# Kernel tuning notes

Hardware: AMD Instinct MI355X
Metric: run time of the kernel (lower is better)

Reference implementation:

```python
import jax, jax.numpy as jnp
import numpy as np
import math


def setup_inputs() -> dict:
    key = jax.random.key(0)
    k_x, k_q, k_k, k_v, k_o = jax.random.split(key, 5)
    B, S, D_IN, H, D_K, D_V, D_OUT = 1, 4096, 512, 8, 64, 64, 512
    # torch.rand -> uniform[0,1); scaled by 0.02 to keep softmax unsaturated
    scale = 0.02
    return {
        "x": jax.random.normal(k_x, (B, S, D_IN), dtype=jnp.float32),
        "W_q": jax.random.uniform(k_q, (H, D_IN, D_K), dtype=jnp.float32) * scale,
        "W_k": jax.random.uniform(k_k, (H, D_IN, D_K), dtype=jnp.float32) * scale,
        "W_v": jax.random.uniform(k_v, (H, D_IN, D_V), dtype=jnp.float32) * scale,
        "W_o": jax.random.uniform(k_o, (H, D_V, D_OUT), dtype=jnp.float32) * scale,
    }


def reference(x, W_q, W_k, W_v, W_o):
    # x: [B,S,d_in]; W_q/W_k: [H,d_in,d_k]; W_v: [H,d_in,d_v]; W_o: [H,d_v,d_out]
    S = x.shape[-2]
    d_key = W_k.shape[-1]
    Q = jnp.einsum('hjk,blj->bhlk', W_q, x)   # [B,H,S,d_k]
    K = jnp.einsum('hjk,blj->bhlk', W_k, x)   # [B,H,S,d_k]
    V = jnp.einsum('hjk,blj->bhlk', W_v, x)   # [B,H,S,d_v]
    # causal mask: True where masked (strict upper triangle)
    mask = jnp.triu(jnp.ones((S, S), dtype=bool), k=1)  # [S,S]
    scores = jnp.einsum('bhik,bhjk->bhij', Q, K)        # [B,H,S,S]
    scores = jnp.where(mask, -jnp.inf, scores)
    # is_scaled=True: divide by sqrt(d_key) before softmax
    weights = jax.nn.softmax(scores / math.sqrt(d_key), axis=-1)
    weights = jnp.where(mask, 0.0, weights)
    values = jnp.einsum('bhij,bhjv->bhiv', weights, V)  # [B,H,S,d_v]
    return jnp.einsum('hvk,bhlv->blk', W_o, values)     # [B,S,d_out]
```

## Files before the change

### kernel.cpp

```cpp
#include <hip/hip_runtime.h>
#include <hip/hip_bf16.h>
#include <math.h>

#define S_LEN 4096
#define NH    8

typedef __attribute__((ext_vector_type(8))) short bf16x8;
typedef __attribute__((ext_vector_type(4))) short bf16x4;
typedef __attribute__((ext_vector_type(4))) float f32x4;
typedef __attribute__((ext_vector_type(16))) float f32x16;

#define QSCALE 0.18033688011112042f

__device__ __forceinline__ short f2bf(float f) {
    union { float f; unsigned u; } v; v.f = f;
    unsigned r = v.u + 0x7fffu + ((v.u >> 16) & 1u);
    return (short)(r >> 16);
}

__device__ __forceinline__ int pk2(float a, float b) {
    __hip_bfloat162 t = __float22bfloat162_rn(make_float2(a, b));
    union { __hip_bfloat162 h; int i; } u; u.h = t;
    return u.i;
}

__device__ __forceinline__ void gload16(const void* g, void* l) {
    __builtin_amdgcn_global_load_lds(
        (const __attribute__((address_space(1))) unsigned*)g,
        (__attribute__((address_space(3))) unsigned*)l, 16, 0, 0);
}

__device__ __forceinline__ void stage_tile(const short* gsrc, size_t gstride,
                                           short* tile, int t)
{
    const int wave = t >> 6, lane = t & 63;
    const int sub = lane >> 3;
    const int cg  = (lane & 7) ^ sub;
#pragma unroll
    for (int j = 0; j < 2; ++j) {
        const int chunk = wave * 2 + j;
        const int row = chunk * 8 + sub;
        gload16(gsrc + (size_t)row * gstride + cg * 8, tile + chunk * 512);
    }
}

__device__ __forceinline__ bf16x8 frag(const short* tile, int row, int cg) {
    return *(const bf16x8*)&tile[row * 64 + ((cg ^ (row & 7)) << 3)];
}

__device__ __forceinline__ void gemm_mainloop_512(
    const short* __restrict__ Arow, const short* __restrict__ Brow,
    short* As, short* Bs, f32x4 acc[4], int t)
{
    const int wave = t >> 6, lane = t & 63, n16 = lane & 15, quad = lane >> 4;
    stage_tile(Arow, 512, As, t);
    stage_tile(Brow, 512, Bs, t);
    __syncthreads();
    for (int c = 0; c < 8; ++c) {
        const int cur = c & 1;
        if (c < 7) {
            stage_tile(Arow + (c + 1) * 64, 512, As + (1 - cur) * 4096, t);
            stage_tile(Brow + (c + 1) * 64, 512, Bs + (1 - cur) * 4096, t);
        }
        const short* as = As + cur * 4096;
        const short* bs = Bs + cur * 4096;
#pragma unroll
        for (int kh = 0; kh < 2; ++kh) {
            const bf16x8 a = frag(as, wave * 16 + n16, kh * 4 + quad);
#pragma unroll
            for (int nt = 0; nt < 4; ++nt) {
                const bf16x8 b = frag(bs, nt * 16 + n16, kh * 4 + quad);
                acc[nt] = __builtin_amdgcn_mfma_f32_16x16x32_bf16(a, b, acc[nt], 0, 0, 0);
            }
        }
        __syncthreads();
    }
}

__global__ __launch_bounds__(256) void prep_kernel(
    const float* __restrict__ x,
    const float* __restrict__ Wq, const float* __restrict__ Wk,
    const float* __restrict__ Wv, const float* __restrict__ Wo,
    short* __restrict__ xb, short* __restrict__ Wqkvt, short* __restrict__ Wot)
{
    __shared__ short T[64 * 66];
    const int b = blockIdx.x, t = threadIdx.x;
    if (b < 1024) {
        const size_t idx = (size_t)b * 2048 + t * 8;
        const float4 a = *(const float4*)&x[idx];
        const float4 c = *(const float4*)&x[idx + 4];
        bf16x8 o;
        o[0] = f2bf(a.x); o[1] = f2bf(a.y); o[2] = f2bf(a.z); o[3] = f2bf(a.w);
        o[4] = f2bf(c.x); o[5] = f2bf(c.y); o[6] = f2bf(c.z); o[7] = f2bf(c.w);
        *(bf16x8*)&xb[idx] = o;
        return;
    }
    const int c4 = (t & 15) * 4, rsub = t >> 4;
    const int orow = t >> 2, oc16 = (t & 3) * 16;
    if (b < 1216) {
        const int jj = b - 1024, g = jj >> 3, kb = jj & 7;
        const int which = g >> 3, h = g & 7;
        const float* W = ((which == 0) ? Wq : (which == 1) ? Wk : Wv) + (size_t)h * 512 * 64;
#pragma unroll
        for (int p = 0; p < 4; ++p) {
            const int row = p * 16 + rsub;
            const float4 v = *(const float4*)&W[(size_t)(kb * 64 + row) * 64 + c4];
            T[(c4 + 0) * 66 + row] = f2bf(v.x);
            T[(c4 + 1) * 66 + row] = f2bf(v.y);
            T[(c4 + 2) * 66 + row] = f2bf(v.z);
            T[(c4 + 3) * 66 + row] = f2bf(v.w);
        }
        __syncthreads();
        short* O = &Wqkvt[((size_t)g * 64 + orow) * 512 + kb * 64];
        *(bf16x8*)&O[oc16]     = *(const bf16x8*)&T[orow * 66 + oc16];
        *(bf16x8*)&O[oc16 + 8] = *(const bf16x8*)&T[orow * 66 + oc16 + 8];
    } else {
        const int jj = b - 1216, h = jj >> 3, nb = jj & 7;
        const float* W = Wo + (size_t)h * 64 * 512;
#pragma unroll
        for (int p = 0; p < 4; ++p) {
            const int row = p * 16 + rsub;
            const float4 v = *(const float4*)&W[(size_t)row * 512 + nb * 64 + c4];
            T[(c4 + 0) * 66 + row] = f2bf(v.x);
            T[(c4 + 1) * 66 + row] = f2bf(v.y);
            T[(c4 + 2) * 66 + row] = f2bf(v.z);
            T[(c4 + 3) * 66 + row] = f2bf(v.w);
        }
        __syncthreads();
        short* O = &Wot[((size_t)nb * 64 + orow) * 512 + h * 64];
        *(bf16x8*)&O[oc16]     = *(const bf16x8*)&T[orow * 66 + oc16];
        *(bf16x8*)&O[oc16 + 8] = *(const bf16x8*)&T[orow * 66 + oc16 + 8];
    }
}

__global__ __launch_bounds__(256) void qkv_gemm_kernel(
    const short* __restrict__ xb, const short* __restrict__ Wqkvt,
    short* __restrict__ Qg, short* __restrict__ Kg, short* __restrict__ Vtg)
{
    __shared__ short smem[16384];
    short* As = smem;
    short* Bs = smem + 8192;
    const int sblk = blockIdx.x, g = blockIdx.y;
    const int which = g >> 3, h = g & 7;
    const int t = threadIdx.x;
    const int wave = t >> 6, lane = t & 63, n16 = lane & 15, quad = lane >> 4;

    f32x4 acc[4] = {{0,0,0,0},{0,0,0,0},{0,0,0,0},{0,0,0,0}};
    gemm_mainloop_512(xb + (size_t)sblk * 64 * 512, Wqkvt + (size_t)g * 64 * 512,
                      As, Bs, acc, t);

    if (which < 2) {
        const float scale = (which == 0) ? QSCALE : 1.0f;
        short* O = ((which == 0) ? Qg : Kg) + (size_t)h * S_LEN * 64;
#pragma unroll
        for (int nt = 0; nt < 4; ++nt)
#pragma unroll
            for (int r = 0; r < 4; ++r) {
                const int s = sblk * 64 + wave * 16 + quad * 4 + r;
                O[(size_t)s * 64 + nt * 16 + n16] = f2bf(acc[nt][r] * scale);
            }
    } else {
        __syncthreads();
        short* Tr = smem;
#pragma unroll
        for (int nt = 0; nt < 4; ++nt)
#pragma unroll
            for (int r = 0; r < 4; ++r)
                Tr[(nt * 16 + n16) * 66 + wave * 16 + quad * 4 + r] = f2bf(acc[nt][r]);
        __syncthreads();
        short* O = Vtg + (size_t)h * 64 * S_LEN + sblk * 64;
        const int r4 = t >> 2, c16 = (t & 3) * 16;
        *(bf16x8*)&O[(size_t)r4 * S_LEN + c16]     = *(const bf16x8*)&Tr[r4 * 66 + c16];
        *(bf16x8*)&O[(size_t)r4 * S_LEN + c16 + 8] = *(const bf16x8*)&Tr[r4 * 66 + c16 + 8];
    }
}

__global__ __launch_bounds__(256) void out_gemm_kernel(
    const short* __restrict__ vals, const short* __restrict__ Wot, float* __restrict__ out)
{
    __shared__ short smem[16384];
    short* As = smem;
    short* Bs = smem + 8192;
    const int sblk = blockIdx.x, g = blockIdx.y;
    const int t = threadIdx.x;
    const int wave = t >> 6, lane = t & 63, n16 = lane & 15, quad = lane >> 4;

    f32x4 acc[4] = {{0,0,0,0},{0,0,0,0},{0,0,0,0},{0,0,0,0}};
    gemm_mainloop_512(vals + (size_t)sblk * 64 * 512, Wot + (size_t)g * 64 * 512,
                      As, Bs, acc, t);

#pragma unroll
    for (int nt = 0; nt < 4; ++nt)
#pragma unroll
        for (int r = 0; r < 4; ++r) {
            const int s = sblk * 64 + wave * 16 + quad * 4 + r;
            out[(size_t)s * 512 + g * 64 + nt * 16 + n16] = acc[nt][r];
        }
}

__global__ __launch_bounds__(256, 3) void attn_kernel(
    const short* __restrict__ Qg, const short* __restrict__ Kg,
    const short* __restrict__ Vtg, float* __restrict__ Opart, float* __restrict__ Lpart)
{
    __shared__ short Ks[2][4096];
    __shared__ short Vs[2][4096];
    __shared__ short Ps[4 * 32 * 72];

    const int id = blockIdx.x;
    const int h  = id & 7;
    const int c  = 79 - (id >> 3);
    int qs, j;
    if (c < 8)       { qs = c;                   j = 0; }
    else if (c < 24) { qs = 8 + ((c - 8) >> 1);  j = (c - 8) & 1; }
    else if (c < 48) { qs = 16 + (c - 24) / 3;   j = (c - 24) % 3; }
    else             { qs = 24 + ((c - 48) >> 2); j = (c - 48) & 3; }
    const int k0   = j * 16;
    const int kend = min(k0 + 16, 2 * qs + 2);

    const short* Kh  = Kg  + (size_t)h * S_LEN * 64;
    const short* Vth = Vtg + (size_t)h * 64 * S_LEN;

    const int t = threadIdx.x;
    const int wave = t >> 6, lane = t & 63, l31 = lane & 31, half = lane >> 5;
    const int qg = qs * 128 + wave * 32 + l31;

    const short* Qr = Qg + (size_t)h * S_LEN * 64 + (size_t)qg * 64;
    bf16x8 bq[4];
#pragma unroll
    for (int kc = 0; kc < 4; ++kc)
        bq[kc] = *(const bf16x8*)&Qr[kc * 16 + half * 8];

    f32x16 oacc[2];
#pragma unroll
    for (int r = 0; r < 16; ++r) { oacc[0][r] = 0.f; oacc[1][r] = 0.f; }
    float lsum = 0.f;
    short* Pw = Ps + wave * (32 * 72);

    stage_tile(Kh + (size_t)k0 * 64 * 64, 64, Ks[0], t);
    stage_tile(Vth + k0 * 64, S_LEN, Vs[0], t);
    __syncthreads();

    for (int kb = k0; kb < kend; ++kb) {
        const int cur = (kb - k0) & 1;
        if (kb + 1 < kend) {
            stage_tile(Kh + (size_t)(kb + 1) * 64 * 64, 64, Ks[1 - cur], t);
            stage_tile(Vth + (kb + 1) * 64, S_LEN, Vs[1 - cur], t);
        }

        f32x16 sc[2];
#pragma unroll
        for (int r = 0; r < 16; ++r) { sc[0][r] = 0.f; sc[1][r] = 0.f; }
#pragma unroll
        for (int kc = 0; kc < 4; ++kc) {
            const bf16x8 a0 = frag(Ks[cur], l31,      kc * 2 + half);
            const bf16x8 a1 = frag(Ks[cur], 32 + l31, kc * 2 + half);
            sc[0] = __builtin_amdgcn_mfma_f32_32x32x16_bf16(a0, bq[kc], sc[0], 0, 0, 0);
            sc[1] = __builtin_amdgcn_mfma_f32_32x32x16_bf16(a1, bq[kc], sc[1], 0, 0, 0);
        }

        if (kb * 64 + 63 > qg) {
#pragma unroll
            for (int mt = 0; mt < 2; ++mt)
#pragma unroll
                for (int r = 0; r < 16; ++r) {
                    const int key = kb * 64 + mt * 32 + (r & 3) + 8 * (r >> 2) + 4 * half;
                    if (key > qg) sc[mt][r] = -1e30f;
                }
        }

#pragma unroll
        for (int mt = 0; mt < 2; ++mt)
#pragma unroll
            for (int g2 = 0; g2 < 4; ++g2) {
                const float p0 = __builtin_amdgcn_exp2f(sc[mt][4 * g2 + 0]);
                const float p1 = __builtin_amdgcn_exp2f(sc[mt][4 * g2 + 1]);
                const float p2 = __builtin_amdgcn_exp2f(sc[mt][4 * g2 + 2]);
                const float p3 = __builtin_amdgcn_exp2f(sc[mt][4 * g2 + 3]);
                lsum += (p0 + p1) + (p2 + p3);
                int2 w; w.x = pk2(p0, p1); w.y = pk2(p2, p3);
                *(int2*)&Pw[l31 * 72 + mt * 32 + g2 * 8 + half * 4] = w;
            }
        __builtin_amdgcn_wave_barrier();

#pragma unroll
        for (int kc = 0; kc < 4; ++kc) {
            const bf16x8 bp = *(const bf16x8*)&Pw[l31 * 72 + kc * 16 + half * 8];
            const bf16x8 a0 = frag(Vs[cur], l31,      kc * 2 + half);
            const bf16x8 a1 = frag(Vs[cur], 32 + l31, kc * 2 + half);
            oacc[0] = __builtin_amdgcn_mfma_f32_32x32x16_bf16(a0, bp, oacc[0], 0, 0, 0);
            oacc[1] = __builtin_amdgcn_mfma_f32_32x32x16_bf16(a1, bp, oacc[1], 0, 0, 0);
        }
        __builtin_amdgcn_wave_barrier();
        __syncthreads();
    }

    lsum += __shfl_xor(lsum, 32);

    float* tileO = Opart + (size_t)(h * 80 + c) * (64 * 128);
    float* tileL = Lpart + (h * 80 + c) * 128;
    if (half == 0) tileL[wave * 32 + l31] = lsum;
#pragma unroll
    for (int mt = 0; mt < 2; ++mt)
#pragma unroll
        for (int r = 0; r < 16; ++r) {
            const int v = mt * 32 + (r & 3) + 8 * (r >> 2) + 4 * half;
            tileO[(v << 7) + wave * 32 + l31] = oacc[mt][r];
        }
}

__global__ __launch_bounds__(256) void combine_norm_kernel(
    const float* __restrict__ Opart, const float* __restrict__ Lpart,
    short* __restrict__ vals)
{
    __shared__ short T[128 * 66];
    const int id = blockIdx.x;
    const int h = id & 7, qs = id >> 3;
    int c0, nj;
    if (qs < 8)       { c0 = qs;                nj = 1; }
    else if (qs < 16) { c0 = 8 + 2 * (qs - 8);  nj = 2; }
    else if (qs < 24) { c0 = 24 + 3 * (qs - 16); nj = 3; }
    else              { c0 = 48 + 4 * (qs - 24); nj = 4; }
    const int base = h * 80 + c0;

    const int t = threadIdx.x;
    const int q0 = (t & 31) * 4;
    const int vr = t >> 5;

    f32x4 L = {0, 0, 0, 0};
    for (int j = 0; j < nj; ++j)
        L += *(const f32x4*)&Lpart[(base + j) * 128 + q0];
    const f32x4 inv = {1.f / L[0], 1.f / L[1], 1.f / L[2], 1.f / L[3]};

#pragma unroll
    for (int pass = 0; pass < 8; ++pass) {
        const int v = vr + pass * 8;
        f32x4 s = {0, 0, 0, 0};
        for (int j = 0; j < nj; ++j)
            s += *(const f32x4*)&Opart[(size_t)(base + j) * 8192 + (v << 7) + q0];
        T[(q0 + 0) * 66 + v] = f2bf(s[0] * inv[0]);
        T[(q0 + 1) * 66 + v] = f2bf(s[1] * inv[1]);
        T[(q0 + 2) * 66 + v] = f2bf(s[2] * inv[2]);
        T[(q0 + 3) * 66 + v] = f2bf(s[3] * inv[3]);
    }
    __syncthreads();
    const int q = t >> 1, vh = (t & 1) * 32;
    const size_t row = (size_t)(qs * 128 + q) * 512 + h * 64 + vh;
#pragma unroll
    for (int u = 0; u < 4; ++u)
        *(bf16x8*)&vals[row + u * 8] = *(const bf16x8*)&T[q * 66 + vh + u * 8];
}

extern "C" void kernel_launch(void* const* d_in, const int* in_sizes, int n_in,
                              void* d_out, int out_size, void* d_ws, size_t ws_size,
                              hipStream_t stream)
{
    const float* x  = (const float*)d_in[0];
    const float* Wq = (const float*)d_in[1];
    const float* Wk = (const float*)d_in[2];
    const float* Wv = (const float*)d_in[3];
    const float* Wo = (const float*)d_in[4];
    float* out = (float*)d_out;

    short* xb    = (short*)d_ws;
    short* Wqkvt = xb + 2097152;
    short* Wot   = Wqkvt + 786432;
    short* Qg    = Wot + 262144;
    short* Kg    = Qg + 2097152;
    short* Vtg   = Kg + 2097152;
    short* vals  = Vtg + 2097152;
    float* Opart = (float*)(vals + 2097152);
    float* Lpart = Opart + (size_t)640 * 8192;

    prep_kernel<<<1280, 256, 0, stream>>>(x, Wq, Wk, Wv, Wo, xb, Wqkvt, Wot);
    qkv_gemm_kernel<<<dim3(64, 24), 256, 0, stream>>>(xb, Wqkvt, Qg, Kg, Vtg);
    attn_kernel<<<640, 256, 0, stream>>>(Qg, Kg, Vtg, Opart, Lpart);
    combine_norm_kernel<<<256, 256, 0, stream>>>(Opart, Lpart, vals);
    out_gemm_kernel<<<dim3(64, 8), 256, 0, stream>>>(vals, Wot, out);
}
```

Before: 137.6 us.

## Replace syncthreads with split barriers and vmcnt waits; compute row sums via MFMA

```diff
diff --git a/kernel.cpp b/kernel.cpp
--- a/kernel.cpp
+++ b/kernel.cpp
@@ -12,6 +12,9 @@
 
 #define QSCALE 0.18033688011112042f
 
+#define WAIT_VM4 0x0F74
+#define WAIT_VM0 0x0F70
+
 __device__ __forceinline__ short f2bf(float f) {
     union { float f; unsigned u; } v; v.f = f;
     unsigned r = v.u + 0x7fffu + ((v.u >> 16) & 1u);
@@ -55,13 +58,17 @@
     const int wave = t >> 6, lane = t & 63, n16 = lane & 15, quad = lane >> 4;
     stage_tile(Arow, 512, As, t);
     stage_tile(Brow, 512, Bs, t);
-    __syncthreads();
     for (int c = 0; c < 8; ++c) {
         const int cur = c & 1;
+        __builtin_amdgcn_s_barrier();
         if (c < 7) {
             stage_tile(Arow + (c + 1) * 64, 512, As + (1 - cur) * 4096, t);
             stage_tile(Brow + (c + 1) * 64, 512, Bs + (1 - cur) * 4096, t);
-        }
+            __builtin_amdgcn_s_waitcnt(WAIT_VM4);
+        } else {
+            __builtin_amdgcn_s_waitcnt(WAIT_VM0);
+        }
+        __builtin_amdgcn_s_barrier();
         const short* as = As + cur * 4096;
         const short* bs = Bs + cur * 4096;
 #pragma unroll
@@ -73,7 +80,6 @@
                 acc[nt] = __builtin_amdgcn_mfma_f32_16x16x32_bf16(a, b, acc[nt], 0, 0, 0);
             }
         }
-        __syncthreads();
     }
 }
 
@@ -230,56 +236,73 @@
     for (int kc = 0; kc < 4; ++kc)
         bq[kc] = *(const bf16x8*)&Qr[kc * 16 + half * 8];
 
-    f32x16 oacc[2];
-#pragma unroll
-    for (int r = 0; r < 16; ++r) { oacc[0][r] = 0.f; oacc[1][r] = 0.f; }
-    float lsum = 0.f;
+    bf16x8 ones;
+#pragma unroll
+    for (int i = 0; i < 8; ++i) ones[i] = (short)0x3F80;
+
+    f32x16 z16;
+#pragma unroll
+    for (int r = 0; r < 16; ++r) z16[r] = 0.f;
+
+    f32x16 oacc[2], lacc;
+#pragma unroll
+    for (int r = 0; r < 16; ++r) { oacc[0][r] = 0.f; oacc[1][r] = 0.f; lacc[r] = 0.f; }
     short* Pw = Ps + wave * (32 * 72);
 
     stage_tile(Kh + (size_t)k0 * 64 * 64, 64, Ks[0], t);
     stage_tile(Vth + k0 * 64, S_LEN, Vs[0], t);
-    __syncthreads();
 
     for (int kb = k0; kb < kend; ++kb) {
         const int cur = (kb - k0) & 1;
+        __builtin_amdgcn_s_barrier();
         if (kb + 1 < kend) {
             stage_tile(Kh + (size_t)(kb + 1) * 64 * 64, 64, Ks[1 - cur], t);
             stage_tile(Vth + (kb + 1) * 64, S_LEN, Vs[1 - cur], t);
-        }
-
-        f32x16 sc[2];
-#pragma unroll
-        for (int r = 0; r < 16; ++r) { sc[0][r] = 0.f; sc[1][r] = 0.f; }
-#pragma unroll
-        for (int kc = 0; kc < 4; ++kc) {
+            __builtin_amdgcn_s_waitcnt(WAIT_VM4);
+        } else {
+            __builtin_amdgcn_s_waitcnt(WAIT_VM0);
+        }
+        __builtin_amdgcn_s_barrier();
+
+        f32x16 sc0, sc1;
+        {
+            const bf16x8 a0 = frag(Ks[cur], l31,      half);
+            const bf16x8 a1 = frag(Ks[cur], 32 + l31, half);
+            sc0 = __builtin_amdgcn_mfma_f32_32x32x16_bf16(a0, bq[0], z16, 0, 0, 0);
+            sc1 = __builtin_amdgcn_mfma_f32_32x32x16_bf16(a1, bq[0], z16, 0, 0, 0);
+        }
+#pragma unroll
+        for (int kc = 1; kc < 4; ++kc) {
             const bf16x8 a0 = frag(Ks[cur], l31,      kc * 2 + half);
             const bf16x8 a1 = frag(Ks[cur], 32 + l31, kc * 2 + half);
-            sc[0] = __builtin_amdgcn_mfma_f32_32x32x16_bf16(a0, bq[kc], sc[0], 0, 0, 0);
-            sc[1] = __builtin_amdgcn_mfma_f32_32x32x16_bf16(a1, bq[kc], sc[1], 0, 0, 0);
+            sc0 = __builtin_amdgcn_mfma_f32_32x32x16_bf16(a0, bq[kc], sc0, 0, 0, 0);
+            sc1 = __builtin_amdgcn_mfma_f32_32x32x16_bf16(a1, bq[kc], sc1, 0, 0, 0);
         }
 
         if (kb * 64 + 63 > qg) {
 #pragma unroll
-            for (int mt = 0; mt < 2; ++mt)
-#pragma unroll
-                for (int r = 0; r < 16; ++r) {
-                    const int key = kb * 64 + mt * 32 + (r & 3) + 8 * (r >> 2) + 4 * half;
-                    if (key > qg) sc[mt][r] = -1e30f;
-                }
-        }
-
-#pragma unroll
-        for (int mt = 0; mt < 2; ++mt)
-#pragma unroll
-            for (int g2 = 0; g2 < 4; ++g2) {
-                const float p0 = __builtin_amdgcn_exp2f(sc[mt][4 * g2 + 0]);
-                const float p1 = __builtin_amdgcn_exp2f(sc[mt][4 * g2 + 1]);
-                const float p2 = __builtin_amdgcn_exp2f(sc[mt][4 * g2 + 2]);
-                const float p3 = __builtin_amdgcn_exp2f(sc[mt][4 * g2 + 3]);
-                lsum += (p0 + p1) + (p2 + p3);
-                int2 w; w.x = pk2(p0, p1); w.y = pk2(p2, p3);
-                *(int2*)&Pw[l31 * 72 + mt * 32 + g2 * 8 + half * 4] = w;
+            for (int r = 0; r < 16; ++r) {
+                const int keyb = kb * 64 + (r & 3) + 8 * (r >> 2) + 4 * half;
+                if (keyb > qg)      sc0[r] = -1e30f;
+                if (keyb + 32 > qg) sc1[r] = -1e30f;
             }
+        }
+
+#pragma unroll
+        for (int g2 = 0; g2 < 4; ++g2) {
+            int2 w;
+            w.x = pk2(__builtin_amdgcn_exp2f(sc0[4 * g2 + 0]),
+                      __builtin_amdgcn_exp2f(sc0[4 * g2 + 1]));
+            w.y = pk2(__builtin_amdgcn_exp2f(sc0[4 * g2 + 2]),
+                      __builtin_amdgcn_exp2f(sc0[4 * g2 + 3]));
+            *(int2*)&Pw[l31 * 72 + g2 * 8 + half * 4] = w;
+            int2 w2;
+            w2.x = pk2(__builtin_amdgcn_exp2f(sc1[4 * g2 + 0]),
+                       __builtin_amdgcn_exp2f(sc1[4 * g2 + 1]));
+            w2.y = pk2(__builtin_amdgcn_exp2f(sc1[4 * g2 + 2]),
+                       __builtin_amdgcn_exp2f(sc1[4 * g2 + 3]));
+            *(int2*)&Pw[l31 * 72 + 32 + g2 * 8 + half * 4] = w2;
+        }
         __builtin_amdgcn_wave_barrier();
 
 #pragma unroll
@@ -289,22 +312,20 @@
             const bf16x8 a1 = frag(Vs[cur], 32 + l31, kc * 2 + half);
             oacc[0] = __builtin_amdgcn_mfma_f32_32x32x16_bf16(a0, bp, oacc[0], 0, 0, 0);
             oacc[1] = __builtin_amdgcn_mfma_f32_32x32x16_bf16(a1, bp, oacc[1], 0, 0, 0);
+            lacc    = __builtin_amdgcn_mfma_f32_32x32x16_bf16(ones, bp, lacc, 0, 0, 0);
         }
         __builtin_amdgcn_wave_barrier();
-        __syncthreads();
-    }
-
-    lsum += __shfl_xor(lsum, 32);
+    }
 
     float* tileO = Opart + (size_t)(h * 80 + c) * (64 * 128);
     float* tileL = Lpart + (h * 80 + c) * 128;
-    if (half == 0) tileL[wave * 32 + l31] = lsum;
+    if (half == 0) tileL[wave * 32 + l31] = lacc[0];
 #pragma unroll
     for (int mt = 0; mt < 2; ++mt)
 #pragma unroll
         for (int r = 0; r < 16; ++r) {
             const int v = mt * 32 + (r & 3) + 8 * (r >> 2) + 4 * half;
-            tileO[(v << 7) + wave * 32 + l31] = oacc[mt][r];
+            tileO[(v << 7) + wave * 32 + l31] = (mt ? oacc[1][r] : oacc[0][r]);
         }
 }
 
@@ -316,8 +337,8 @@
     const int id = blockIdx.x;
     const int h = id & 7, qs = id >> 3;
     int c0, nj;
-    if (qs < 8)       { c0 = qs;                nj = 1; }
-    else if (qs < 16) { c0 = 8 + 2 * (qs - 8);  nj = 2; }
+    if (qs < 8)       { c0 = qs;                 nj = 1; }
+    else if (qs < 16) { c0 = 8 + 2 * (qs - 8);   nj = 2; }
     else if (qs < 24) { c0 = 24 + 3 * (qs - 16); nj = 3; }
     else              { c0 = 48 + 4 * (qs - 24); nj = 4; }
     const int base = h * 80 + c0;
```

Measured after the change: 135.2 us, median of 2. Within noise of the previous version (-1.7%).
